# Optimization experiments

Hardware: AMD Instinct MI355X
Metric: run time of the kernel (lower is better)

Reference implementation:

```python
import jax, jax.numpy as jnp
import numpy as np

HEAD_SIZE = 8
MODEL_SIZE = 512
K_SIZE = 64
V_SIZE = 64
B, L = 4, 2048


def setup_inputs() -> dict:
    key = jax.random.key(0)
    ks = jax.random.split(key, 12)
    s = 0.02
    inp = {
        "q": jax.random.normal(ks[0], (B, L, MODEL_SIZE), jnp.float32),
        "k": jax.random.normal(ks[1], (B, L, MODEL_SIZE), jnp.float32),
        "v": jax.random.normal(ks[2], (B, L, MODEL_SIZE), jnp.float32),
        "attn_mask": jax.random.randint(ks[3], (B, L, L), 0, 2).astype(jnp.bool_),
        "Wq": jax.random.normal(ks[4], (K_SIZE, MODEL_SIZE), jnp.float32) * s,
        "bq": jnp.zeros((K_SIZE,), jnp.float32),
        "Wk": jax.random.normal(ks[5], (K_SIZE, MODEL_SIZE), jnp.float32) * s,
        "bk": jnp.zeros((K_SIZE,), jnp.float32),
        "Wv": jax.random.normal(ks[6], (V_SIZE, MODEL_SIZE), jnp.float32) * s,
        "bv": jnp.zeros((V_SIZE,), jnp.float32),
        "Wp": jax.random.normal(ks[7], (MODEL_SIZE, HEAD_SIZE * V_SIZE), jnp.float32) * s,
        "bp": jnp.zeros((MODEL_SIZE,), jnp.float32),
    }
    return inp


def reference(q, k, v, attn_mask, Wq, bq, Wk, bk, Wv, bv, Wp, bp):
    # Original module applies the same linear_q/k/v to head-repeated tensors,
    # so every head is identical; compute once and tile (exactly equal math).
    temperature = jnp.asarray(MODEL_SIZE, q.dtype) ** 0.5  # note: sqrt(model_size), not sqrt(k_size)
    qp = jnp.einsum('bld,kd->blk', q, Wq) + bq  # (B, Lq, k_size)
    kp = jnp.einsum('bld,kd->blk', k, Wk) + bk  # (B, Lk, k_size)
    vp = jnp.einsum('bld,kd->blk', v, Wv) + bv  # (B, Lk, v_size)
    attn = jnp.einsum('bqd,bkd->bqk', qp, kp) / temperature  # (B, Lq, Lk)
    attn = jnp.where(attn_mask, -jnp.inf, attn)
    attn = jax.nn.softmax(attn, axis=-1)  # dropout is identity at eval
    out = jnp.einsum('bqk,bkd->bqd', attn, vp)  # (B, Lq, v_size)
    out = jnp.tile(out, (1, 1, HEAD_SIZE))  # concat of identical per-head outputs
    out = jnp.einsum('blh,mh->blm', out, Wp) + bp  # (B, Lq, model_size)
    return out
```

## Files before the change

kernel.cpp:

```cpp
#include <hip/hip_runtime.h>

#define B_ 4
#define L_ 2048
#define MD_ 512
#define KV_ 64
#define NKT_ (L_ / 64)
#define KSPLIT 4
#define NT_ (NKT_ / KSPLIT)

typedef unsigned short u16;
typedef unsigned char u8;
typedef unsigned int u32;
typedef unsigned long long u64;
typedef __attribute__((ext_vector_type(8))) short bf16x8;
typedef __attribute__((ext_vector_type(4))) float f32x4;
typedef __attribute__((ext_vector_type(4))) u32 u32x4;
typedef __attribute__((ext_vector_type(4))) u16 u16x4;

#define INV_T 0.044194173824159216f

static __device__ __forceinline__ u16 f2bf(float x) {
  u32 u = __float_as_uint(x);
  return (u16)((u + 0x7FFFu + ((u >> 16) & 1u)) >> 16);
}
static __device__ __forceinline__ f32x4 zero4() {
  f32x4 z = {0.f, 0.f, 0.f, 0.f};
  return z;
}
static __device__ __forceinline__ f32x4 mfma16(bf16x8 a, bf16x8 b, f32x4 c) {
  return __builtin_amdgcn_mfma_f32_16x16x32_bf16(a, b, c, 0, 0, 0);
}

__global__ __launch_bounds__(256) void mha_prep(
    const float* __restrict__ Wq, const float* __restrict__ Wk,
    const float* __restrict__ Wv, const float* __restrict__ bq,
    const float* __restrict__ bk, const float* __restrict__ bv,
    const float* __restrict__ Wp, u16* __restrict__ WtT,
    float* __restrict__ bqkv, u16* __restrict__ WpT) {
  int t = blockIdx.x * 256 + threadIdx.x;
  if (t < 3 * 64 * 512) {
    int p = t >> 15, c = (t >> 9) & 63, d = t & 511;
    const float* W = (p == 0) ? Wq : ((p == 1) ? Wk : Wv);
    WtT[(p * 64 + c) * 520 + d] = f2bf(W[c * 512 + d]);
  } else if (t < 3 * 64 * 512 + 512 * 64) {
    int i = t - 3 * 64 * 512;
    int m = i >> 6, d = i & 63;
    float s = 0.f;
#pragma unroll
    for (int h = 0; h < 8; h++) s += Wp[m * 512 + h * 64 + d];
    WpT[m * 72 + d] = f2bf(s);
  } else if (t < 3 * 64 * 512 + 512 * 64 + 192) {
    int j = t - (3 * 64 * 512 + 512 * 64);
    int p = j >> 6;
    const float* bb = (p == 0) ? bq : ((p == 1) ? bk : bv);
    bqkv[j] = bb[j & 63];
  }
}

__global__ __launch_bounds__(256) void mha_proj(
    const float* __restrict__ q, const float* __restrict__ k,
    const float* __restrict__ v, const u16* __restrict__ WtT,
    const float* __restrict__ bqkv, u16* __restrict__ qp,
    u16* __restrict__ kp, u16* __restrict__ vpt) {
  __shared__ __align__(16) u16 X[3][32][520];
  __shared__ __align__(16) u16 Xv[32][72];
  const int tid = threadIdx.x;
  const int r0 = blockIdx.x * 32;
#pragma unroll 4
  for (int i = 0; i < 48; i++) {
    int e = tid + i * 256;
    int p = e >> 12, r = (e >> 7) & 31, dq = (e & 127) << 2;
    const float* src = (p == 0) ? q : ((p == 1) ? k : v);
    f32x4 xv = *(const f32x4*)(src + (size_t)(r0 + r) * 512 + dq);
    u16x4 w4 = {f2bf(xv[0]), f2bf(xv[1]), f2bf(xv[2]), f2bf(xv[3])};
    *(u16x4*)&X[p][r][dq] = w4;
  }
  __syncthreads();
  const int w = tid >> 6, l = tid & 63, g = l >> 4, li = l & 15;
  const int mt = w & 1, half = w >> 1;
  f32x4 acc[6];
#pragma unroll
  for (int i = 0; i < 6; i++) acc[i] = zero4();

  if (half == 0) {
#pragma unroll 4
    for (int ks = 0; ks < 16; ks++) {
      const int ko = g * 8 + ks * 32;
      bf16x8 a0 = *(const bf16x8*)&X[0][mt * 16 + li][ko];
      bf16x8 a1 = *(const bf16x8*)&X[1][mt * 16 + li][ko];
      acc[0] = mfma16(a0, *(const bf16x8*)(WtT + (0 * 64 + 0 + li) * 520 + ko), acc[0]);
      acc[1] = mfma16(a0, *(const bf16x8*)(WtT + (0 * 64 + 16 + li) * 520 + ko), acc[1]);
      acc[2] = mfma16(a0, *(const bf16x8*)(WtT + (0 * 64 + 32 + li) * 520 + ko), acc[2]);
      acc[3] = mfma16(a0, *(const bf16x8*)(WtT + (0 * 64 + 48 + li) * 520 + ko), acc[3]);
      acc[4] = mfma16(a1, *(const bf16x8*)(WtT + (1 * 64 + 0 + li) * 520 + ko), acc[4]);
      acc[5] = mfma16(a1, *(const bf16x8*)(WtT + (1 * 64 + 16 + li) * 520 + ko), acc[5]);
    }
  } else {
#pragma unroll 4
    for (int ks = 0; ks < 16; ks++) {
      const int ko = g * 8 + ks * 32;
      bf16x8 a1 = *(const bf16x8*)&X[1][mt * 16 + li][ko];
      bf16x8 a2 = *(const bf16x8*)&X[2][mt * 16 + li][ko];
      acc[0] = mfma16(a1, *(const bf16x8*)(WtT + (1 * 64 + 32 + li) * 520 + ko), acc[0]);
      acc[1] = mfma16(a1, *(const bf16x8*)(WtT + (1 * 64 + 48 + li) * 520 + ko), acc[1]);
      acc[2] = mfma16(a2, *(const bf16x8*)(WtT + (2 * 64 + 0 + li) * 520 + ko), acc[2]);
      acc[3] = mfma16(a2, *(const bf16x8*)(WtT + (2 * 64 + 16 + li) * 520 + ko), acc[3]);
      acc[4] = mfma16(a2, *(const bf16x8*)(WtT + (2 * 64 + 32 + li) * 520 + ko), acc[4]);
      acc[5] = mfma16(a2, *(const bf16x8*)(WtT + (2 * 64 + 48 + li) * 520 + ko), acc[5]);
    }
  }
#pragma unroll
  for (int i = 0; i < 6; i++) {
    int nt = half * 6 + i;
    int p = nt >> 2, c4 = nt & 3;
    float bias = bqkv[nt * 16 + li];
#pragma unroll
    for (int j = 0; j < 4; j++) {
      int row = r0 + mt * 16 + g * 4 + j;
      u16 val = f2bf(acc[i][j] + bias);
      if (p == 0)
        qp[(size_t)row * 64 + c4 * 16 + li] = val;
      else if (p == 1)
        kp[(size_t)row * 64 + c4 * 16 + li] = val;
      else
        Xv[mt * 16 + g * 4 + j][c4 * 16 + li] = val;
    }
  }
  __syncthreads();
  {
    int d = tid >> 2, ch = tid & 3;
    size_t bb_ = (size_t)(r0 >> 11), kk = (size_t)(r0 & 2047);
    u16 tmp[8];
#pragma unroll
    for (int r = 0; r < 8; r++) tmp[r] = Xv[ch * 8 + r][d];
    *(bf16x8*)(vpt + (bb_ * 64 + d) * 2048 + kk + ch * 8) = *(bf16x8*)tmp;
  }
}

#define KB(CT) (Klds[CT])
#define VB(CT) (Vlds[CT])

#define STAGE_LOAD(KT)                                                         \
  do {                                                                         \
    size_t kb_ = brow + (size_t)(KT) * 64;                                     \
    kreg0 = *(const u32x4*)(kp + (kb_ + sr0) * 64 + (l & 7) * 8);              \
    kreg1 = *(const u32x4*)(kp + (kb_ + sr0 + 8) * 64 + (l & 7) * 8);          \
    vreg0 = *(const u32x4*)(vpt + ((size_t)b * 64 + sr0) * 2048 +              \
                            (size_t)(KT) * 64 + (l & 7) * 8);                  \
    vreg1 = *(const u32x4*)(vpt + ((size_t)b * 64 + sr0 + 8) * 2048 +          \
                            (size_t)(KT) * 64 + (l & 7) * 8);                  \
  } while (0)

#define STAGE_WRITE(CT)                                                        \
  do {                                                                         \
    *(u32x4*)(KB(CT) + swz0) = kreg0;                                          \
    *(u32x4*)(KB(CT) + swz0 + 1024) = kreg1;                                   \
    *(u32x4*)(VB(CT) + swz0) = vreg0;                                          \
    *(u32x4*)(VB(CT) + swz0 + 1024) = vreg1;                                   \
  } while (0)

#define LOADM(M, KT)                                                           \
  do {                                                                         \
    _Pragma("unroll") for (int nt_ = 0; nt_ < 4; nt_++) {                      \
      M[nt_] = *(const u32x4*)(mrow + (size_t)(KT) * 64 + nt_ * 16);           \
    }                                                                          \
  } while (0)

#define COMPUTE(CT, M)                                                         \
  do {                                                                         \
    f32x4 sacc[4];                                                             \
    _Pragma("unroll") for (int nt = 0; nt < 4; nt++) {                         \
      bf16x8 kf0 = *(const bf16x8*)(KB(CT) + (nt * 16 + li) * 128 + cA);       \
      bf16x8 kf1 = *(const bf16x8*)(KB(CT) + (nt * 16 + li) * 128 + cB);       \
      sacc[nt] = mfma16(kf0, qf0, zero4());                                    \
      sacc[nt] = mfma16(kf1, qf1, sacc[nt]);                                   \
    }                                                                          \
    _Pragma("unroll") for (int nt = 0; nt < 4; nt++) {                         \
      float pv[4];                                                             \
      _Pragma("unroll") for (int r = 0; r < 4; r++) {                          \
        float ex = __expf(sacc[nt][r] * INV_T);                                \
        pv[r] = M[nt][r] ? 0.f : ex;                                           \
        rsl += pv[r];                                                          \
      }                                                                        \
      u16x4 pk = {f2bf(pv[0]), f2bf(pv[1]), f2bf(pv[2]), f2bf(pv[3])};         \
      *(u16x4*)&Plds[w][li][nt * 16 + 4 * g] = pk;                             \
    }                                                                          \
    _Pragma("unroll") for (int ks = 0; ks < 2; ks++) {                         \
      bf16x8 pa = *(const bf16x8*)&Plds[w][li][ks * 32 + g * 8];               \
      int vcol = (ks == 0) ? cA : cB;                                          \
      _Pragma("unroll") for (int dt = 0; dt < 4; dt++) {                       \
        bf16x8 vb = *(const bf16x8*)(VB(CT) + (dt * 16 + li) * 128 + vcol);    \
        o[dt] = mfma16(pa, vb, o[dt]);                                         \
      }                                                                        \
    }                                                                          \
  } while (0)

#define BODY(T, MCUR, MNXT)                                                    \
  do {                                                                         \
    if ((T) + 1 < NT_) {                                                       \
      STAGE_LOAD(kt0 + (T) + 1);                                               \
      LOADM(MNXT, kt0 + (T) + 1);                                              \
    }                                                                          \
    COMPUTE((T) & 1, MCUR);                                                    \
    if ((T) + 1 < NT_) {                                                       \
      STAGE_WRITE(((T) & 1) ^ 1);                                              \
      __syncthreads();                                                         \
    }                                                                          \
  } while (0)

__global__ __launch_bounds__(256, 2) void mha_attn(
    const u16* __restrict__ qp, const u16* __restrict__ kp,
    const u16* __restrict__ vpt, const int* __restrict__ mask,
    u16* __restrict__ po, float* __restrict__ pl) {
  __shared__ __align__(16) char Klds[2][8192];
  __shared__ __align__(16) char Vlds[2][8192];
  __shared__ __align__(16) u16 Plds[4][16][72];
  const int tid = threadIdx.x;
  const int w = tid >> 6, l = tid & 63, g = l >> 4, li = l & 15;
  const int b = blockIdx.y;
  const int q0 = blockIdx.x * 64;
  const int s = blockIdx.z;
  const size_t brow = (size_t)b * L_;
  const int kt0 = s * NT_;

  const int sr0 = w * 16 + (l >> 3);
  const int swz0 = sr0 * 128 + (((l & 7) * 16) ^ ((l & 7) << 4 & 0x70) ^
                                (((sr0 & 7) << 4)) ^ ((l & 7) * 16));
  const int swz0_ = sr0 * 128 + (((l & 7) * 16) ^ ((sr0 & 7) << 4));
  (void)swz0;
#undef STAGE_WRITE
#define STAGE_WRITE(CT)                                                        \
  do {                                                                         \
    *(u32x4*)(KB(CT) + swz0_) = kreg0;                                         \
    *(u32x4*)(KB(CT) + swz0_ + 1024) = kreg1;                                  \
    *(u32x4*)(VB(CT) + swz0_) = vreg0;                                         \
    *(u32x4*)(VB(CT) + swz0_ + 1024) = vreg1;                                  \
  } while (0)

  const int cA = (g * 16) ^ ((li & 7) << 4);
  const int cB = (g * 16 + 64) ^ ((li & 7) << 4);

  bf16x8 qf0 = *(const bf16x8*)(qp + (brow + q0 + w * 16 + li) * 64 + g * 8);
  bf16x8 qf1 =
      *(const bf16x8*)(qp + (brow + q0 + w * 16 + li) * 64 + g * 8 + 32);

  f32x4 o[4];
#pragma unroll
  for (int i = 0; i < 4; i++) o[i] = zero4();
  float rsl = 0.f;

  const u32* mrow =
      (const u32*)mask + (brow + q0 + w * 16 + li) * (size_t)L_ + 4 * g;

  u32x4 kreg0, kreg1, vreg0, vreg1;
  u32x4 mA[4], mB[4];

  STAGE_LOAD(kt0);
  LOADM(mA, kt0);
  STAGE_WRITE(0);
  __syncthreads();

  BODY(0, mA, mB);
  BODY(1, mB, mA);
  BODY(2, mA, mB);
  BODY(3, mB, mA);
  BODY(4, mA, mB);
  BODY(5, mB, mA);
  BODY(6, mA, mB);
  BODY(7, mB, mA);

  rsl += __shfl_xor(rsl, 16);
  rsl += __shfl_xor(rsl, 32);
#pragma unroll
  for (int j = 0; j < 4; j++) {
    size_t r = brow + q0 + w * 16 + g * 4 + j;
    size_t base = (r * KSPLIT + s) * 64;
#pragma unroll
    for (int dt = 0; dt < 4; dt++) po[base + dt * 16 + li] = f2bf(o[dt][j]);
  }
  if (l < 16) pl[(brow + q0 + w * 16 + l) * KSPLIT + s] = rsl;
}

__global__ __launch_bounds__(256) void mha_comb(const u16* __restrict__ po,
                                                const float* __restrict__ pl,
                                                u16* __restrict__ aout) {
  int id = blockIdx.x * 256 + threadIdx.x;
  int r = id >> 6, d = id & 63;
  float L = 0.f, acc = 0.f;
#pragma unroll
  for (int i = 0; i < KSPLIT; i++) {
    L += pl[r * KSPLIT + i];
    u16 u = po[((size_t)(r * KSPLIT + i)) * 64 + d];
    acc += __uint_as_float((u32)u << 16);
  }
  aout[(size_t)r * 64 + d] = f2bf(acc / L);
}

__global__ __launch_bounds__(128) void mha_fin(const u16* __restrict__ aout,
                                               const u16* __restrict__ WpT,
                                               const float* __restrict__ bp,
                                               float* __restrict__ out) {
  const int tid = threadIdx.x;
  const int w = tid >> 6, l = tid & 63, g = l >> 4, li = l & 15;
  const size_t r0 = (size_t)blockIdx.x * 32;
  const u16* ar = aout + (r0 + w * 16 + li) * 64;
  bf16x8 a0 = *(const bf16x8*)(ar + g * 8);
  bf16x8 a1 = *(const bf16x8*)(ar + g * 8 + 32);
#pragma unroll 4
  for (int nt = 0; nt < 32; nt++) {
    bf16x8 b0 = *(const bf16x8*)(WpT + (nt * 16 + li) * 72 + g * 8);
    bf16x8 b1 = *(const bf16x8*)(WpT + (nt * 16 + li) * 72 + g * 8 + 32);
    f32x4 acc = zero4();
    acc = mfma16(a0, b0, acc);
    acc = mfma16(a1, b1, acc);
    float bias = bp[nt * 16 + li];
#pragma unroll
    for (int j = 0; j < 4; j++)
      out[(r0 + w * 16 + g * 4 + j) * 512 + nt * 16 + li] = acc[j] + bias;
  }
}

extern "C" void kernel_launch(void* const* d_in, const int* in_sizes, int n_in,
                              void* d_out, int out_size, void* d_ws,
                              size_t ws_size, hipStream_t stream) {
  const float* q = (const float*)d_in[0];
  const float* k = (const float*)d_in[1];
  const float* v = (const float*)d_in[2];
  const int* mask = (const int*)d_in[3];
  const float* Wq = (const float*)d_in[4];
  const float* bq = (const float*)d_in[5];
  const float* Wk = (const float*)d_in[6];
  const float* bk = (const float*)d_in[7];
  const float* Wv = (const float*)d_in[8];
  const float* bv = (const float*)d_in[9];
  const float* Wp = (const float*)d_in[10];
  const float* bp = (const float*)d_in[11];

  char* ws = (char*)d_ws;
  u16* qp = (u16*)(ws + 0);
  u16* kp = (u16*)(ws + 1048576);
  u16* vpt = (u16*)(ws + 2097152);
  u16* aout = (u16*)(ws + 3145728);
  u16* WtT = (u16*)(ws + 4194304);
  float* bqkv = (float*)(ws + 4393984);
  u16* WpT = (u16*)(ws + 4394752);
  u16* po = (u16*)(ws + 4468736);
  float* pl = (float*)(ws + 8663040);

  mha_prep<<<dim3(513), dim3(256), 0, stream>>>(Wq, Wk, Wv, bq, bk, bv, Wp,
                                                WtT, bqkv, WpT);
  mha_proj<<<dim3(256), dim3(256), 0, stream>>>(q, k, v, WtT, bqkv, qp, kp,
                                                vpt);
  mha_attn<<<dim3(32, 4, KSPLIT), dim3(256), 0, stream>>>(qp, kp, vpt, mask,
                                                          po, pl);
  mha_comb<<<dim3(2048), dim3(256), 0, stream>>>(po, pl, aout);
  mha_fin<<<dim3(256), dim3(128), 0, stream>>>(aout, WpT, bp, (float*)d_out);
}
```

Measured before the change: 55.20 us.

## Pre-pack the int mask into a bitmask in a separate kernel before attention

Adds a mask-packing kernel that uses wavefront ballots to turn the 32-bit int attention mask into 64-bit words holding bits laid out for the attention kernel's MFMA tiles. The attention kernel then loads one u64 per row tile instead of four 16-byte vectors, which cuts its global-load traffic and register use. The full int mask still has to be read once by the new kernel, so the total bytes read only fall if the attention kernel had been reading the mask inefficiently or was latency-bound on it. The change also adds one more launch.

```diff
diff --git a/kernel.cpp b/kernel.cpp
--- a/kernel.cpp
+++ b/kernel.cpp
@@ -54,6 +54,30 @@
     int p = j >> 6;
     const float* bb = (p == 0) ? bq : ((p == 1) ? bk : bv);
     bqkv[j] = bb[j & 63];
+  }
+}
+
+__global__ __launch_bounds__(256) void mha_mask(const int* __restrict__ mask,
+                                                u64* __restrict__ pkm) {
+  const int tid = threadIdx.x;
+  const int l = tid & 63;
+  const size_t wid = (blockIdx.x * 256 + tid) >> 6;
+  const size_t NW = 1024 * 4;
+  const size_t TOT = (size_t)B_ * L_ * L_;
+  for (size_t base = wid * 256; base < TOT; base += NW * 256) {
+    u32x4 m = *(const u32x4*)(mask + base + l * 4);
+    u64 bal[4];
+#pragma unroll
+    for (int j = 0; j < 4; j++) bal[j] = __ballot(m[j] != 0);
+    if (l < 4) {
+      u64 pk = 0;
+#pragma unroll
+      for (int j = 0; j < 4; j++)
+        pk |= ((bal[j] >> (l * 16)) & 0xFFFFull) << (16 * j);
+      size_t R = base >> 11;
+      int kt0 = (int)((base & 2047) >> 6);
+      pkm[R * 32 + kt0 + l] = pk;
+    }
   }
 }
 
@@ -159,14 +183,7 @@
     *(u32x4*)(VB(CT) + swz0 + 1024) = vreg1;                                   \
   } while (0)
 
-#define LOADM(M, KT)                                                           \
-  do {                                                                         \
-    _Pragma("unroll") for (int nt_ = 0; nt_ < 4; nt_++) {                      \
-      M[nt_] = *(const u32x4*)(mrow + (size_t)(KT) * 64 + nt_ * 16);           \
-    }                                                                          \
-  } while (0)
-
-#define COMPUTE(CT, M)                                                         \
+#define COMPUTE(CT, PK)                                                        \
   do {                                                                         \
     f32x4 sacc[4];                                                             \
     _Pragma("unroll") for (int nt = 0; nt < 4; nt++) {                         \
@@ -179,11 +196,11 @@
       float pv[4];                                                             \
       _Pragma("unroll") for (int r = 0; r < 4; r++) {                          \
         float ex = __expf(sacc[nt][r] * INV_T);                                \
-        pv[r] = M[nt][r] ? 0.f : ex;                                           \
+        pv[r] = (((PK) >> (r * 16 + nt * 4 + g)) & 1) ? 0.f : ex;              \
         rsl += pv[r];                                                          \
       }                                                                        \
-      u16x4 pk = {f2bf(pv[0]), f2bf(pv[1]), f2bf(pv[2]), f2bf(pv[3])};         \
-      *(u16x4*)&Plds[w][li][nt * 16 + 4 * g] = pk;                             \
+      u16x4 pk_ = {f2bf(pv[0]), f2bf(pv[1]), f2bf(pv[2]), f2bf(pv[3])};        \
+      *(u16x4*)&Plds[w][li][nt * 16 + 4 * g] = pk_;                            \
     }                                                                          \
     _Pragma("unroll") for (int ks = 0; ks < 2; ks++) {                         \
       bf16x8 pa = *(const bf16x8*)&Plds[w][li][ks * 32 + g * 8];               \
@@ -195,13 +212,13 @@
     }                                                                          \
   } while (0)
 
-#define BODY(T, MCUR, MNXT)                                                    \
+#define BODY(T, PKC, PKN)                                                      \
   do {                                                                         \
     if ((T) + 1 < NT_) {                                                       \
       STAGE_LOAD(kt0 + (T) + 1);                                               \
-      LOADM(MNXT, kt0 + (T) + 1);                                              \
-    }                                                                          \
-    COMPUTE((T) & 1, MCUR);                                                    \
+      PKN = prow[kt0 + (T) + 1];                                               \
+    }                                                                          \
+    COMPUTE((T) & 1, PKC);                                                     \
     if ((T) + 1 < NT_) {                                                       \
       STAGE_WRITE(((T) & 1) ^ 1);                                              \
       __syncthreads();                                                         \
@@ -210,7 +227,7 @@
 
 __global__ __launch_bounds__(256, 2) void mha_attn(
     const u16* __restrict__ qp, const u16* __restrict__ kp,
-    const u16* __restrict__ vpt, const int* __restrict__ mask,
+    const u16* __restrict__ vpt, const u64* __restrict__ pkm,
     u16* __restrict__ po, float* __restrict__ pl) {
   __shared__ __align__(16) char Klds[2][8192];
   __shared__ __align__(16) char Vlds[2][8192];
@@ -224,18 +241,7 @@
   const int kt0 = s * NT_;
 
   const int sr0 = w * 16 + (l >> 3);
-  const int swz0 = sr0 * 128 + (((l & 7) * 16) ^ ((l & 7) << 4 & 0x70) ^
-                                (((sr0 & 7) << 4)) ^ ((l & 7) * 16));
-  const int swz0_ = sr0 * 128 + (((l & 7) * 16) ^ ((sr0 & 7) << 4));
-  (void)swz0;
-#undef STAGE_WRITE
-#define STAGE_WRITE(CT)                                                        \
-  do {                                                                         \
-    *(u32x4*)(KB(CT) + swz0_) = kreg0;                                         \
-    *(u32x4*)(KB(CT) + swz0_ + 1024) = kreg1;                                  \
-    *(u32x4*)(VB(CT) + swz0_) = vreg0;                                         \
-    *(u32x4*)(VB(CT) + swz0_ + 1024) = vreg1;                                  \
-  } while (0)
+  const int swz0 = sr0 * 128 + (((l & 7) * 16) ^ ((sr0 & 7) << 4));
 
   const int cA = (g * 16) ^ ((li & 7) << 4);
   const int cB = (g * 16 + 64) ^ ((li & 7) << 4);
@@ -249,25 +255,24 @@
   for (int i = 0; i < 4; i++) o[i] = zero4();
   float rsl = 0.f;
 
-  const u32* mrow =
-      (const u32*)mask + (brow + q0 + w * 16 + li) * (size_t)L_ + 4 * g;
+  const u64* prow = pkm + (brow + q0 + w * 16 + li) * 32;
 
   u32x4 kreg0, kreg1, vreg0, vreg1;
-  u32x4 mA[4], mB[4];
+  u64 pkA, pkB;
 
   STAGE_LOAD(kt0);
-  LOADM(mA, kt0);
+  pkA = prow[kt0];
   STAGE_WRITE(0);
   __syncthreads();
 
-  BODY(0, mA, mB);
-  BODY(1, mB, mA);
-  BODY(2, mA, mB);
-  BODY(3, mB, mA);
-  BODY(4, mA, mB);
-  BODY(5, mB, mA);
-  BODY(6, mA, mB);
-  BODY(7, mB, mA);
+  BODY(0, pkA, pkB);
+  BODY(1, pkB, pkA);
+  BODY(2, pkA, pkB);
+  BODY(3, pkB, pkA);
+  BODY(4, pkA, pkB);
+  BODY(5, pkB, pkA);
+  BODY(6, pkA, pkB);
+  BODY(7, pkB, pkA);
 
   rsl += __shfl_xor(rsl, 16);
   rsl += __shfl_xor(rsl, 32);
@@ -346,12 +351,14 @@
   u16* WpT = (u16*)(ws + 4394752);
   u16* po = (u16*)(ws + 4468736);
   float* pl = (float*)(ws + 8663040);
+  u64* pkm = (u64*)(ws + 8794112);
 
   mha_prep<<<dim3(513), dim3(256), 0, stream>>>(Wq, Wk, Wv, bq, bk, bv, Wp,
                                                 WtT, bqkv, WpT);
+  mha_mask<<<dim3(1024), dim3(256), 0, stream>>>(mask, pkm);
   mha_proj<<<dim3(256), dim3(256), 0, stream>>>(q, k, v, WtT, bqkv, qp, kp,
                                                 vpt);
-  mha_attn<<<dim3(32, 4, KSPLIT), dim3(256), 0, stream>>>(qp, kp, vpt, mask,
+  mha_attn<<<dim3(32, 4, KSPLIT), dim3(256), 0, stream>>>(qp, kp, vpt, pkm,
                                                           po, pl);
   mha_comb<<<dim3(2048), dim3(256), 0, stream>>>(po, pl, aout);
   mha_fin<<<dim3(256), dim3(128), 0, stream>>>(aout, WpT, bp, (float*)d_out);
```

Measured after the change: 63.97 us. 15.9% more time.
